# Performance work log

Hardware: AMD Instinct MI355X
Metric: run time of the kernel (lower is better)

The kernel has to match this reference:

```python
import jax, jax.numpy as jnp
import numpy as np

B, S, D_IN, D_OUT = 4, 2048, 768, 768

def setup_inputs() -> dict:
    key = jax.random.key(0)
    kx, kq, kk, kv = jax.random.split(key, 4)
    scale = 1.0 / np.sqrt(D_IN)
    return {
        "x": jax.random.normal(kx, (B, S, D_IN), dtype=jnp.float32),
        "Wq": jax.random.normal(kq, (D_OUT, D_IN), dtype=jnp.float32) * scale,
        "Wk": jax.random.normal(kk, (D_OUT, D_IN), dtype=jnp.float32) * scale,
        "Wv": jax.random.normal(kv, (D_OUT, D_IN), dtype=jnp.float32) * scale,
    }

def reference(x, Wq, Wk, Wv):
    # torch Linear: y = x @ W.T  (W is [d_out, d_in])
    q = jnp.einsum('bsd,od->bso', x, Wq)
    k = jnp.einsum('bsd,od->bso', x, Wk)
    v = jnp.einsum('bsd,od->bso', x, Wv)
    scores = jnp.einsum('bqo,bko->bqk', q, k)  # [B,S,S]
    causal = jnp.tril(jnp.ones((scores.shape[1], scores.shape[2]), dtype=bool))
    neg_inf = jnp.array(-jnp.inf, dtype=scores.dtype)
    scores = jnp.where(causal, scores, neg_inf)
    inv_sqrt_d = jnp.asarray(1.0 / np.sqrt(q.shape[-1]), dtype=scores.dtype)
    weights = jax.nn.softmax(scores * inv_sqrt_d, axis=-1)
    # dropout p=0.0 -> identity
    return jnp.einsum('bqk,bko->bqo', weights, v)
```

## Files before the change

kernel.cpp:

```cpp
#include <hip/hip_runtime.h>
#include <hip/hip_bf16.h>
#include <cstdint>
#include <cstddef>


typedef __attribute__((ext_vector_type(8))) short short8;
typedef __attribute__((ext_vector_type(4))) float f32x4;

#define GPTR(p) (const __attribute__((address_space(1))) void*)(p)
#define LPTR(p) (__attribute__((address_space(3))) void*)(p)
#define MFMA16(a8, b8, c) c = __builtin_amdgcn_mfma_f32_16x16x32_bf16(a8, b8, c, 0, 0, 0)

constexpr int CB = 4, CS = 2048, CD = 768;
constexpr int CBS = CB * CS;

typedef const __attribute__((address_space(3))) char* lds_cp;

__device__ __forceinline__ short8 ds_read128(const __hip_bfloat16* p) {
    short8 r;
    lds_cp a = (lds_cp)p;
    asm volatile("ds_read_b128 %0, %1" : "=v"(r) : "v"(a));
    return r;
}

__device__ inline unsigned short f2bf_bits(float v) {
    __hip_bfloat16 h = __float2bfloat16(v);
    unsigned short u;
    __builtin_memcpy(&u, &h, 2);
    return u;
}

__device__ inline ushort4 cvt4(float4 f) {
    ushort4 u;
    u.x = f2bf_bits(f.x); u.y = f2bf_bits(f.y);
    u.z = f2bf_bits(f.z); u.w = f2bf_bits(f.w);
    return u;
}

template <int MI>
__device__ __forceinline__ void zero_acc(f32x4 (&acc)[MI][4]) {
#pragma unroll
    for (int i = 0; i < MI; ++i)
#pragma unroll
        for (int j = 0; j < 4; ++j)
            acc[i][j] = f32x4{0.f, 0.f, 0.f, 0.f};
}

__global__ __launch_bounds__(256) void cvt_all(
    const float4* __restrict__ x,  const float4* __restrict__ wq,
    const float4* __restrict__ wk, const float4* __restrict__ wv,
    ushort4* __restrict__ x16, ushort4* __restrict__ w16,
    float4* __restrict__ rsum4)
{
    constexpr int NX = CBS * CD / 4;
    constexpr int NW = CD * CD / 4;
    constexpr int NT = NX + 3 * NW;
    const int i = blockIdx.x * 256 + threadIdx.x;
    if (i < NX) {
        x16[i] = cvt4(x[i]);
    } else if (i < NT) {
        const int j = i - NX;
        if (j < NW)            w16[j] = cvt4(wq[j]);
        else if (j < 2 * NW)   w16[j] = cvt4(wk[j - NW]);
        else                   w16[j] = cvt4(wv[j - 2 * NW]);
    } else {
        const int j = i - NT;
        rsum4[j] = float4{0.f, 0.f, 0.f, 0.f};
    }
}

__device__ __forceinline__ void gemm256_core(
    const __hip_bfloat16* __restrict__ A,
    const __hip_bfloat16* __restrict__ B,
    __hip_bfloat16* As, __hip_bfloat16* Bs,
    int m0, int n0, int K, int nkt,
    f32x4 (&acc)[8][4])
{
    const int t   = threadIdx.x;
    const int w   = t >> 6;
    const int l   = t & 63;
    const int lq  = l >> 4;
    const int lm  = l & 15;
    const int wm  = w >> 2;
    const int wn  = w & 3;
    const int lm7 = lm & 7;
    const int c0  = (lq ^ lm7) << 3;
    const int c1  = c0 ^ 32;

    const int rr0   = t >> 3;
    const int gp8   = (t & 7) << 3;
    const int g8    = (((t & 7) ^ (rr0 & 7)) << 3);
    const int rowBa = ((rr0 & 32) << 1) | (rr0 & 31);

    const __hip_bfloat16* Aori = A + (size_t)m0 * K;
    const __hip_bfloat16* Bori = B + (size_t)n0 * K;

    auto stage = [&](int reg, int bufT, int kt) {
        const int kc = kt * 64 + g8;
        const __hip_bfloat16* s0;
        __hip_bfloat16* d;
        if (reg == 0) {
            s0 = Aori + (size_t)rr0 * K + kc;
            d  = As + bufT * 16384 + rr0 * 64 + gp8;
        } else if (reg == 2) {
            s0 = Aori + (size_t)(64 + rr0) * K + kc;
            d  = As + bufT * 16384 + (64 + rr0) * 64 + gp8;
        } else if (reg == 3) {
            s0 = Bori + (size_t)rowBa * K + kc;
            d  = Bs + bufT * 16384 + rowBa * 64 + gp8;
        } else {
            s0 = Bori + (size_t)(32 + rowBa) * K + kc;
            d  = Bs + bufT * 16384 + (32 + rowBa) * 64 + gp8;
        }
        __builtin_amdgcn_global_load_lds(GPTR(s0), LPTR(d), 16, 0, 0);
        __builtin_amdgcn_global_load_lds(GPTR(s0 + (size_t)128 * K), LPTR(d + 8192), 16, 0, 0);
    };

    stage(0, 0, 0); stage(1, 0, 0); stage(2, 0, 0); stage(3, 0, 0);
    stage(0, 1, 1); stage(1, 1, 1); stage(2, 1, 1);
    asm volatile("s_waitcnt vmcnt(6)" ::: "memory");
    __builtin_amdgcn_s_barrier();

    for (int kt = 0; kt < nkt; ++kt) {
        const int buf = kt & 1;
        const __hip_bfloat16* Ab = As + buf * 16384 + wm * 8192 + lm * 64;
        const __hip_bfloat16* Bb = Bs + buf * 16384 + (wn >> 1) * 8192 + (wn & 1) * 4096 + lm * 64;
        short8 af[4][2], bf[2][2];

#pragma unroll
        for (int i = 0; i < 4; ++i) {
            af[i][0] = ds_read128(&Ab[i * 1024 + c0]);
            af[i][1] = ds_read128(&Ab[i * 1024 + c1]);
        }
#pragma unroll
        for (int j = 0; j < 2; ++j) {
            bf[j][0] = ds_read128(&Bb[j * 1024 + c0]);
            bf[j][1] = ds_read128(&Bb[j * 1024 + c1]);
        }
        if (kt + 1 < nkt) stage(3, buf ^ 1, kt + 1);
        __builtin_amdgcn_s_barrier();
        asm volatile("s_waitcnt lgkmcnt(0)");
        __builtin_amdgcn_sched_barrier(0);
        __builtin_amdgcn_s_setprio(1);
#pragma unroll
        for (int i = 0; i < 4; ++i)
#pragma unroll
            for (int j = 0; j < 2; ++j) {
                MFMA16(af[i][0], bf[j][0], acc[i][j]);
                MFMA16(af[i][1], bf[j][1], acc[i][j]);
            }
        __builtin_amdgcn_s_setprio(0);
        __builtin_amdgcn_s_barrier();

#pragma unroll
        for (int j = 0; j < 2; ++j) {
            bf[j][0] = ds_read128(&Bb[(2 + j) * 1024 + c0]);
            bf[j][1] = ds_read128(&Bb[(2 + j) * 1024 + c1]);
        }
        if (kt + 2 < nkt) stage(0, buf, kt + 2);
        __builtin_amdgcn_s_barrier();
        asm volatile("s_waitcnt lgkmcnt(0)");
        __builtin_amdgcn_sched_barrier(0);
        __builtin_amdgcn_s_setprio(1);
#pragma unroll
        for (int i = 0; i < 4; ++i)
#pragma unroll
            for (int j = 0; j < 2; ++j) {
                MFMA16(af[i][0], bf[j][0], acc[i][2 + j]);
                MFMA16(af[i][1], bf[j][1], acc[i][2 + j]);
            }
        __builtin_amdgcn_s_setprio(0);
        __builtin_amdgcn_s_barrier();

#pragma unroll
        for (int i = 0; i < 4; ++i) {
            af[i][0] = ds_read128(&Ab[(4 + i) * 1024 + c0]);
            af[i][1] = ds_read128(&Ab[(4 + i) * 1024 + c1]);
        }
        if (kt + 2 < nkt) stage(1, buf, kt + 2);
        __builtin_amdgcn_s_barrier();
        asm volatile("s_waitcnt lgkmcnt(0)");
        __builtin_amdgcn_sched_barrier(0);
        __builtin_amdgcn_s_setprio(1);
#pragma unroll
        for (int i = 0; i < 4; ++i)
#pragma unroll
            for (int j = 0; j < 2; ++j) {
                MFMA16(af[i][0], bf[j][0], acc[4 + i][2 + j]);
                MFMA16(af[i][1], bf[j][1], acc[4 + i][2 + j]);
            }
        __builtin_amdgcn_s_setprio(0);
        __builtin_amdgcn_s_barrier();

#pragma unroll
        for (int j = 0; j < 2; ++j) {
            bf[j][0] = ds_read128(&Bb[j * 1024 + c0]);
            bf[j][1] = ds_read128(&Bb[j * 1024 + c1]);
        }
        if (kt + 2 < nkt) stage(2, buf, kt + 2);
        __builtin_amdgcn_s_barrier();
        asm volatile("s_waitcnt lgkmcnt(0)");
        __builtin_amdgcn_sched_barrier(0);
        __builtin_amdgcn_s_setprio(1);
#pragma unroll
        for (int i = 0; i < 4; ++i)
#pragma unroll
            for (int j = 0; j < 2; ++j) {
                MFMA16(af[i][0], bf[j][0], acc[4 + i][j]);
                MFMA16(af[i][1], bf[j][1], acc[4 + i][j]);
            }
        __builtin_amdgcn_s_setprio(0);
        if (kt + 2 < nkt) {
            asm volatile("s_waitcnt vmcnt(6)" ::: "memory");
        } else if (kt + 1 < nkt) {
            asm volatile("s_waitcnt vmcnt(0)" ::: "memory");
        }
        __builtin_amdgcn_s_barrier();
    }
}

__global__ __launch_bounds__(512, 2) void qk256_gemm(
    const __hip_bfloat16* __restrict__ x16,
    const __hip_bfloat16* __restrict__ w16,
    __hip_bfloat16* __restrict__ q16,
    __hip_bfloat16* __restrict__ k16)
{
    __shared__ __align__(16) __hip_bfloat16 As[2 * 16384];
    __shared__ __align__(16) __hip_bfloat16 Bs[2 * 16384];

    const int id   = blockIdx.x;
    const int mi   = id / 6;
    const int r    = id % 6;
    const int proj = r / 3;
    const int nj   = r % 3;
    const int m0 = mi * 256, n0 = nj * 256;

    f32x4 acc[8][4];
    zero_acc<8>(acc);
    gemm256_core(x16, w16 + (size_t)proj * CD * CD, As, Bs, m0, n0, CD, CD / 64, acc);

    __hip_bfloat16* C = proj ? k16 : q16;
    const int t = threadIdx.x, w = t >> 6, l = t & 63, lq = l >> 4, lm = l & 15;
    const int wm = w >> 2, wn = w & 3;
#pragma unroll
    for (int i = 0; i < 8; ++i)
#pragma unroll
        for (int j = 0; j < 4; ++j) {
            const int n = n0 + wn * 64 + j * 16 + lm;
#pragma unroll
            for (int r2 = 0; r2 < 4; ++r2) {
                const int m = m0 + wm * 128 + i * 16 + lq * 4 + r2;
                C[(size_t)m * CD + n] = __float2bfloat16(acc[i][j][r2]);
            }
        }
}

__global__ __launch_bounds__(512, 2) void scores_vt_gemm(
    const __hip_bfloat16* __restrict__ q16,
    const __hip_bfloat16* __restrict__ k16,
    const __hip_bfloat16* __restrict__ x16,
    const __hip_bfloat16* __restrict__ w16,
    __hip_bfloat16* __restrict__ sp16,
    __hip_bfloat16* __restrict__ vt16,
    float* __restrict__ rowsum,
    float scale)
{
    __shared__ __align__(16) __hip_bfloat16 As[2 * 16384];
    __shared__ __align__(16) __hip_bfloat16 Bs[2 * 16384];

    const int id = blockIdx.x;
    const __hip_bfloat16 *A, *B;
    int m0, n0, b;
    const bool is_sc = (id < 144);
    if (is_sc) {
        b = id / 36;
        const int tt = id % 36;
        int mi = (int)((sqrtf(8.f * tt + 1.f) - 1.f) * 0.5f);
        while ((mi + 1) * (mi + 2) / 2 <= tt) ++mi;
        while (mi * (mi + 1) / 2 > tt) --mi;
        const int nj = tt - mi * (mi + 1) / 2;
        m0 = mi * 256; n0 = nj * 256;
        A = q16 + (size_t)b * CS * CD;
        B = k16 + (size_t)b * CS * CD;
    } else {
        int r = id - 144;
        b = r / 24; r %= 24;
        m0 = (r >> 3) * 256;
        n0 = (r & 7) * 256;
        A = w16 + (size_t)2 * CD * CD;
        B = x16 + (size_t)b * CS * CD;
    }

    f32x4 acc[8][4];
    zero_acc<8>(acc);
    gemm256_core(A, B, As, Bs, m0, n0, CD, CD / 64, acc);

    const int t = threadIdx.x, w = t >> 6, l = t & 63, lq = l >> 4, lm = l & 15;
    const int wm = w >> 2, wn = w & 3;

    if (is_sc) {
        __hip_bfloat16* C = sp16 + (size_t)b * CS * CS;
        float* rs = rowsum + (size_t)b * CS;
#pragma unroll
        for (int i = 0; i < 8; ++i) {
            float psum[4] = {0.f, 0.f, 0.f, 0.f};
#pragma unroll
            for (int j = 0; j < 4; ++j) {
                const int n = n0 + wn * 64 + j * 16 + lm;
#pragma unroll
                for (int r2 = 0; r2 < 4; ++r2) {
                    const int m = m0 + wm * 128 + i * 16 + lq * 4 + r2;
                    float e = (n <= m) ? __expf(acc[i][j][r2] * scale) : 0.f;
                    C[(size_t)m * CS + n] = __float2bfloat16(e);
                    psum[r2] += e;
                }
            }
#pragma unroll
            for (int r2 = 0; r2 < 4; ++r2) {
#pragma unroll
                for (int off = 1; off < 16; off <<= 1)
                    psum[r2] += __shfl_xor(psum[r2], off);
                if (lm == 0) {
                    const int m = m0 + wm * 128 + i * 16 + lq * 4 + r2;
                    atomicAdd(&rs[m], psum[r2]);
                }
            }
        }
    } else {
        __hip_bfloat16* C = vt16 + (size_t)b * CD * CS;
#pragma unroll
        for (int i = 0; i < 8; ++i)
#pragma unroll
            for (int j = 0; j < 4; ++j) {
                const int n = n0 + wn * 64 + j * 16 + lm;
#pragma unroll
                for (int r2 = 0; r2 < 4; ++r2) {
                    const int m = m0 + wm * 128 + i * 16 + lq * 4 + r2;
                    C[(size_t)m * CS + n] = __float2bfloat16(acc[i][j][r2]);
                }
            }
    }
}

template <int BM>
__device__ __forceinline__ void gemm_core(
    const __hip_bfloat16* __restrict__ A,
    const __hip_bfloat16* __restrict__ B,
    __hip_bfloat16* As, __hip_bfloat16* Bs,
    int m0, int n0, int K, int kend,
    f32x4 (&acc)[BM / 32][4])
{
    constexpr int AC = BM / 16;
    constexpr int SC = AC + 8;
    constexpr int MI = BM / 32;

    const int t  = threadIdx.x;
    const int w  = t >> 6;
    const int l  = t & 63;
    const int lq = l >> 4;
    const int lm = l & 15;
    const int wm = (w >> 1) * (BM / 2);
    const int wn = (w & 1) * 64;

    const int srow = l >> 2;
    const int scol = (l & 3) * 8;

    auto stage = [&](int buf, int k0) {
#pragma unroll
        for (int ci = 0; ci < SC / 4; ++ci) {
            const int c = ci * 4 + w;
            if (c < AC) {
                __builtin_amdgcn_global_load_lds(
                    GPTR(A + (size_t)(m0 + c * 16 + srow) * K + k0 + scol),
                    LPTR(&As[buf * BM * 32 + c * 512]), 16, 0, 0);
            } else {
                const int c2 = c - AC;
                __builtin_amdgcn_global_load_lds(
                    GPTR(B + (size_t)(n0 + c2 * 16 + srow) * K + k0 + scol),
                    LPTR(&Bs[buf * 128 * 32 + c2 * 512]), 16, 0, 0);
            }
        }
    };

    stage(0, 0);
    asm volatile("s_waitcnt vmcnt(0)" ::: "memory");
    __syncthreads();

    int cur = 0;
    for (int k0 = 0; k0 < kend; k0 += 32) {
        if (k0 + 32 < kend)
            stage(cur ^ 1, k0 + 32);

        short8 af[MI], bf[4];
#pragma unroll
        for (int i = 0; i < MI; ++i)
            af[i] = *(const short8*)&As[cur * BM * 32 + (wm + i * 16 + lm) * 32 + lq * 8];
#pragma unroll
        for (int j = 0; j < 4; ++j)
            bf[j] = *(const short8*)&Bs[cur * 128 * 32 + (wn + j * 16 + lm) * 32 + lq * 8];

#pragma unroll
        for (int i = 0; i < MI; ++i)
#pragma unroll
            for (int j = 0; j < 4; ++j)
                acc[i][j] = __builtin_amdgcn_mfma_f32_16x16x32_bf16(
                    af[i], bf[j], acc[i][j], 0, 0, 0);

        __syncthreads();
        cur ^= 1;
    }
}

__global__ __launch_bounds__(256) void pv_gemm(
    const __hip_bfloat16* __restrict__ sp16,
    const __hip_bfloat16* __restrict__ vt16,
    const float* __restrict__ rowsum,
    float* __restrict__ out)
{
    const int id   = blockIdx.x;
    const int mrev = id / 24;
    int r          = id % 24;
    const int b    = r / 6;
    const int n0   = (r % 6) * 128;
    const int mi   = 31 - mrev;
    const int m0   = mi * 64;
    const int kend = m0 + 64;

    __shared__ __align__(16) __hip_bfloat16 As[2 * 64 * 32];
    __shared__ __align__(16) __hip_bfloat16 Bs[2 * 128 * 32];

    const __hip_bfloat16* A = sp16 + (size_t)b * CS * CS;
    const __hip_bfloat16* B = vt16 + (size_t)b * CD * CS;
    float* Co = out + (size_t)b * CS * CD;
    const float* rs = rowsum + (size_t)b * CS;

    f32x4 acc[2][4];
    zero_acc<2>(acc);
    gemm_core<64>(A, B, As, Bs, m0, n0, CS, kend, acc);

    const int t  = threadIdx.x;
    const int w  = t >> 6;
    const int l  = t & 63;
    const int lq = l >> 4;
    const int lm = l & 15;
    const int wm = (w >> 1) * 32;
    const int wn = (w & 1) * 64;

#pragma unroll
    for (int i = 0; i < 2; ++i) {
        float inv[4];
#pragma unroll
        for (int r2 = 0; r2 < 4; ++r2)
            inv[r2] = 1.0f / rs[m0 + wm + i * 16 + lq * 4 + r2];
#pragma unroll
        for (int j = 0; j < 4; ++j) {
            const int n = n0 + wn + j * 16 + lm;
#pragma unroll
            for (int r2 = 0; r2 < 4; ++r2) {
                const int m = m0 + wm + i * 16 + lq * 4 + r2;
                Co[(size_t)m * CD + n] = acc[i][j][r2] * inv[r2];
            }
        }
    }
}

extern "C" void kernel_launch(void* const* d_in, const int* in_sizes, int n_in,
                              void* d_out, int out_size, void* d_ws, size_t ws_size,
                              hipStream_t stream)
{
    const float* x  = (const float*)d_in[0];
    const float* Wq = (const float*)d_in[1];
    const float* Wk = (const float*)d_in[2];
    const float* Wv = (const float*)d_in[3];
    float* out = (float*)d_out;

    char* ws = (char*)d_ws;
    size_t off = 0;
    auto alloc = [&](size_t bytes) { char* p = ws + off; off += bytes; return p; };

    __hip_bfloat16* x16  = (__hip_bfloat16*)alloc((size_t)CBS * CD * 2);
    __hip_bfloat16* q16  = (__hip_bfloat16*)alloc((size_t)CBS * CD * 2);
    __hip_bfloat16* k16  = (__hip_bfloat16*)alloc((size_t)CBS * CD * 2);
    __hip_bfloat16* vt16 = (__hip_bfloat16*)alloc((size_t)CBS * CD * 2);
    __hip_bfloat16* sp16 = (__hip_bfloat16*)alloc((size_t)CB * CS * CS * 2);
    __hip_bfloat16* w16  = (__hip_bfloat16*)alloc((size_t)3 * CD * CD * 2);
    float*          rsum = (float*)alloc((size_t)CB * CS * sizeof(float));

    constexpr int NCVT_BLK = (CBS * CD + 3 * CD * CD) / 4 / 256 + 8;
    cvt_all<<<NCVT_BLK, 256, 0, stream>>>(
        (const float4*)x, (const float4*)Wq, (const float4*)Wk, (const float4*)Wv,
        (ushort4*)x16, (ushort4*)w16, (float4*)rsum);

    qk256_gemm<<<192, 512, 0, stream>>>(x16, w16, q16, k16);

    scores_vt_gemm<<<240, 512, 0, stream>>>(
        q16, k16, x16, w16, sp16, vt16, rsum, 0.03608439182435161f);

    pv_gemm<<<768, 256, 0, stream>>>(sp16, vt16, rsum, out);
}
```

Measured before the change: 181.5 us.

## Replace PV GEMM with 256-tile split-K kernel using atomics and XCD swizzle

Replaces the 64x128-tile PV kernel with a 256x256-tile kernel that reuses the pipelined gemm256_core. Causal K ranges are split into chunks of 8 k-tiles, and the partial results are combined with float atomicAdd into an output zeroed by an added memset. XCD-aware block swizzling is also applied to the earlier GEMM kernels to improve L2 locality. This trades more data reuse per tile and a balanced 240-block grid for atomic traffic, a memset pass, and nondeterministic summation order.

```diff
diff --git a/kernel.cpp b/kernel.cpp
--- a/kernel.cpp
+++ b/kernel.cpp
@@ -21,6 +21,10 @@
     lds_cp a = (lds_cp)p;
     asm volatile("ds_read_b128 %0, %1" : "=v"(r) : "v"(a));
     return r;
+}
+
+__device__ __forceinline__ int xcd_swz(int bid, int nwg) {
+    return (bid & 7) * (nwg >> 3) + (bid >> 3);
 }
 
 __device__ inline unsigned short f2bf_bits(float v) {
@@ -228,7 +232,7 @@
     __shared__ __align__(16) __hip_bfloat16 As[2 * 16384];
     __shared__ __align__(16) __hip_bfloat16 Bs[2 * 16384];
 
-    const int id   = blockIdx.x;
+    const int id   = xcd_swz(blockIdx.x, 192);
     const int mi   = id / 6;
     const int r    = id % 6;
     const int proj = r / 3;
@@ -268,7 +272,7 @@
     __shared__ __align__(16) __hip_bfloat16 As[2 * 16384];
     __shared__ __align__(16) __hip_bfloat16 Bs[2 * 16384];
 
-    const int id = blockIdx.x;
+    const int id = xcd_swz(blockIdx.x, 240);
     const __hip_bfloat16 *A, *B;
     int m0, n0, b;
     const bool is_sc = (id < 144);
@@ -342,123 +346,53 @@
     }
 }
 
-template <int BM>
-__device__ __forceinline__ void gemm_core(
-    const __hip_bfloat16* __restrict__ A,
-    const __hip_bfloat16* __restrict__ B,
-    __hip_bfloat16* As, __hip_bfloat16* Bs,
-    int m0, int n0, int K, int kend,
-    f32x4 (&acc)[BM / 32][4])
-{
-    constexpr int AC = BM / 16;
-    constexpr int SC = AC + 8;
-    constexpr int MI = BM / 32;
-
-    const int t  = threadIdx.x;
-    const int w  = t >> 6;
-    const int l  = t & 63;
-    const int lq = l >> 4;
-    const int lm = l & 15;
-    const int wm = (w >> 1) * (BM / 2);
-    const int wn = (w & 1) * 64;
-
-    const int srow = l >> 2;
-    const int scol = (l & 3) * 8;
-
-    auto stage = [&](int buf, int k0) {
-#pragma unroll
-        for (int ci = 0; ci < SC / 4; ++ci) {
-            const int c = ci * 4 + w;
-            if (c < AC) {
-                __builtin_amdgcn_global_load_lds(
-                    GPTR(A + (size_t)(m0 + c * 16 + srow) * K + k0 + scol),
-                    LPTR(&As[buf * BM * 32 + c * 512]), 16, 0, 0);
-            } else {
-                const int c2 = c - AC;
-                __builtin_amdgcn_global_load_lds(
-                    GPTR(B + (size_t)(n0 + c2 * 16 + srow) * K + k0 + scol),
-                    LPTR(&Bs[buf * 128 * 32 + c2 * 512]), 16, 0, 0);
-            }
-        }
-    };
-
-    stage(0, 0);
-    asm volatile("s_waitcnt vmcnt(0)" ::: "memory");
-    __syncthreads();
-
-    int cur = 0;
-    for (int k0 = 0; k0 < kend; k0 += 32) {
-        if (k0 + 32 < kend)
-            stage(cur ^ 1, k0 + 32);
-
-        short8 af[MI], bf[4];
-#pragma unroll
-        for (int i = 0; i < MI; ++i)
-            af[i] = *(const short8*)&As[cur * BM * 32 + (wm + i * 16 + lm) * 32 + lq * 8];
-#pragma unroll
-        for (int j = 0; j < 4; ++j)
-            bf[j] = *(const short8*)&Bs[cur * 128 * 32 + (wn + j * 16 + lm) * 32 + lq * 8];
-
-#pragma unroll
-        for (int i = 0; i < MI; ++i)
-#pragma unroll
-            for (int j = 0; j < 4; ++j)
-                acc[i][j] = __builtin_amdgcn_mfma_f32_16x16x32_bf16(
-                    af[i], bf[j], acc[i][j], 0, 0, 0);
-
-        __syncthreads();
-        cur ^= 1;
-    }
-}
-
-__global__ __launch_bounds__(256) void pv_gemm(
+__global__ __launch_bounds__(512, 2) void pv256_gemm(
     const __hip_bfloat16* __restrict__ sp16,
     const __hip_bfloat16* __restrict__ vt16,
     const float* __restrict__ rowsum,
     float* __restrict__ out)
 {
-    const int id   = blockIdx.x;
-    const int mrev = id / 24;
-    int r          = id % 24;
-    const int b    = r / 6;
-    const int n0   = (r % 6) * 128;
-    const int mi   = 31 - mrev;
-    const int m0   = mi * 64;
-    const int kend = m0 + 64;
-
-    __shared__ __align__(16) __hip_bfloat16 As[2 * 64 * 32];
-    __shared__ __align__(16) __hip_bfloat16 Bs[2 * 128 * 32];
-
-    const __hip_bfloat16* A = sp16 + (size_t)b * CS * CS;
-    const __hip_bfloat16* B = vt16 + (size_t)b * CD * CS;
+    __shared__ __align__(16) __hip_bfloat16 As[2 * 16384];
+    __shared__ __align__(16) __hip_bfloat16 Bs[2 * 16384];
+
+    const int id    = xcd_swz(blockIdx.x, 240);
+    const int panel = id / 20;
+    int c           = id % 20;
+    const int b  = panel / 3;
+    const int nj = panel % 3;
+    int mi = 0;
+    while (c >= (mi >> 1) + 1) { c -= (mi >> 1) + 1; ++mi; }
+    const int kt0 = c * 8;
+    const int nkt = min(8, 4 * (mi + 1) - kt0);
+    const int m0 = mi * 256, n0 = nj * 256;
+
+    const __hip_bfloat16* A = sp16 + (size_t)b * CS * CS + kt0 * 64;
+    const __hip_bfloat16* B = vt16 + (size_t)b * CD * CS + kt0 * 64;
+
+    f32x4 acc[8][4];
+    zero_acc<8>(acc);
+    gemm256_core(A, B, As, Bs, m0, n0, CS, nkt, acc);
+
     float* Co = out + (size_t)b * CS * CD;
     const float* rs = rowsum + (size_t)b * CS;
-
-    f32x4 acc[2][4];
-    zero_acc<2>(acc);
-    gemm_core<64>(A, B, As, Bs, m0, n0, CS, kend, acc);
-
-    const int t  = threadIdx.x;
-    const int w  = t >> 6;
-    const int l  = t & 63;
-    const int lq = l >> 4;
-    const int lm = l & 15;
-    const int wm = (w >> 1) * 32;
-    const int wn = (w & 1) * 64;
-
-#pragma unroll
-    for (int i = 0; i < 2; ++i) {
+    const int t = threadIdx.x, w = t >> 6, l = t & 63, lq = l >> 4, lm = l & 15;
+    const int wm = w >> 2, wn = w & 3;
+    const bool single = (mi < 2);
+#pragma unroll
+    for (int i = 0; i < 8; ++i) {
         float inv[4];
 #pragma unroll
         for (int r2 = 0; r2 < 4; ++r2)
-            inv[r2] = 1.0f / rs[m0 + wm + i * 16 + lq * 4 + r2];
+            inv[r2] = 1.0f / rs[m0 + wm * 128 + i * 16 + lq * 4 + r2];
 #pragma unroll
         for (int j = 0; j < 4; ++j) {
-            const int n = n0 + wn + j * 16 + lm;
+            const int n = n0 + wn * 64 + j * 16 + lm;
 #pragma unroll
             for (int r2 = 0; r2 < 4; ++r2) {
-                const int m = m0 + wm + i * 16 + lq * 4 + r2;
-                Co[(size_t)m * CD + n] = acc[i][j][r2] * inv[r2];
+                const int m = m0 + wm * 128 + i * 16 + lq * 4 + r2;
+                const float v = acc[i][j][r2] * inv[r2];
+                if (single) Co[(size_t)m * CD + n] = v;
+                else        atomicAdd(&Co[(size_t)m * CD + n], v);
             }
         }
     }
@@ -486,6 +420,8 @@
     __hip_bfloat16* w16  = (__hip_bfloat16*)alloc((size_t)3 * CD * CD * 2);
     float*          rsum = (float*)alloc((size_t)CB * CS * sizeof(float));
 
+    hipMemsetAsync(out, 0, (size_t)CBS * CD * sizeof(float), stream);
+
     constexpr int NCVT_BLK = (CBS * CD + 3 * CD * CD) / 4 / 256 + 8;
     cvt_all<<<NCVT_BLK, 256, 0, stream>>>(
         (const float4*)x, (const float4*)Wq, (const float4*)Wk, (const float4*)Wv,
@@ -496,5 +432,5 @@
     scores_vt_gemm<<<240, 512, 0, stream>>>(
         q16, k16, x16, w16, sp16, vt16, rsum, 0.03608439182435161f);
 
-    pv_gemm<<<768, 256, 0, stream>>>(sp16, vt16, rsum, out);
-}
+    pv256_gemm<<<240, 512, 0, stream>>>(sp16, vt16, rsum, out);
+}
```

After: 201.8 us. 1.11x slower.

## Hold both A and B fragment halves in registers and swizzle blocks across XCDs

Applied to the files above, without the earlier changes.

The GEMM inner loop now loads both B half-fragments up front and keeps the low and high A fragments in separate registers. This removes the repeated B reloads and one LDS read phase with its barriers per k-tile, and a partial lgkmcnt wait lets the first MFMA block start before all reads finish. Block IDs in both GEMM kernels are also remapped so that neighbouring tiles land on the same XCD, aiming for better L2 reuse. The cost is higher register pressure from the extra fragment arrays, which could hurt occupancy at 512 threads with a minimum of 2 blocks per CU. The last phase also drops a barrier around its staging, which may be fragile.

```diff
diff --git a/kernel.cpp b/kernel.cpp
--- a/kernel.cpp
+++ b/kernel.cpp
@@ -21,6 +21,10 @@
     lds_cp a = (lds_cp)p;
     asm volatile("ds_read_b128 %0, %1" : "=v"(r) : "v"(a));
     return r;
+}
+
+__device__ __forceinline__ int xcd_swz(int bid, int nwg) {
+    return (bid & 7) * (nwg >> 3) + (bid >> 3);
 }
 
 __device__ inline unsigned short f2bf_bits(float v) {
@@ -125,19 +129,40 @@
         const int buf = kt & 1;
         const __hip_bfloat16* Ab = As + buf * 16384 + wm * 8192 + lm * 64;
         const __hip_bfloat16* Bb = Bs + buf * 16384 + (wn >> 1) * 8192 + (wn & 1) * 4096 + lm * 64;
-        short8 af[4][2], bf[2][2];
+        short8 alo[4][2], ahi[4][2], ba[2][2], bb[2][2];
 
 #pragma unroll
         for (int i = 0; i < 4; ++i) {
-            af[i][0] = ds_read128(&Ab[i * 1024 + c0]);
-            af[i][1] = ds_read128(&Ab[i * 1024 + c1]);
+            alo[i][0] = ds_read128(&Ab[i * 1024 + c0]);
+            alo[i][1] = ds_read128(&Ab[i * 1024 + c1]);
         }
 #pragma unroll
         for (int j = 0; j < 2; ++j) {
-            bf[j][0] = ds_read128(&Bb[j * 1024 + c0]);
-            bf[j][1] = ds_read128(&Bb[j * 1024 + c1]);
-        }
+            ba[j][0] = ds_read128(&Bb[j * 1024 + c0]);
+            ba[j][1] = ds_read128(&Bb[j * 1024 + c1]);
+        }
+#pragma unroll
+        for (int j = 0; j < 2; ++j) {
+            bb[j][0] = ds_read128(&Bb[(2 + j) * 1024 + c0]);
+            bb[j][1] = ds_read128(&Bb[(2 + j) * 1024 + c1]);
+        }
+
         if (kt + 1 < nkt) stage(3, buf ^ 1, kt + 1);
+        __builtin_amdgcn_s_barrier();
+        asm volatile("s_waitcnt lgkmcnt(4)");
+        __builtin_amdgcn_sched_barrier(0);
+        __builtin_amdgcn_s_setprio(1);
+#pragma unroll
+        for (int i = 0; i < 4; ++i)
+#pragma unroll
+            for (int j = 0; j < 2; ++j) {
+                MFMA16(alo[i][0], ba[j][0], acc[i][j]);
+                MFMA16(alo[i][1], ba[j][1], acc[i][j]);
+            }
+        __builtin_amdgcn_s_setprio(0);
+        __builtin_amdgcn_s_barrier();
+
+        if (kt + 2 < nkt) stage(0, buf, kt + 2);
         __builtin_amdgcn_s_barrier();
         asm volatile("s_waitcnt lgkmcnt(0)");
         __builtin_amdgcn_sched_barrier(0);
@@ -146,18 +171,18 @@
         for (int i = 0; i < 4; ++i)
 #pragma unroll
             for (int j = 0; j < 2; ++j) {
-                MFMA16(af[i][0], bf[j][0], acc[i][j]);
-                MFMA16(af[i][1], bf[j][1], acc[i][j]);
+                MFMA16(alo[i][0], bb[j][0], acc[i][2 + j]);
+                MFMA16(alo[i][1], bb[j][1], acc[i][2 + j]);
             }
         __builtin_amdgcn_s_setprio(0);
         __builtin_amdgcn_s_barrier();
 
 #pragma unroll
-        for (int j = 0; j < 2; ++j) {
-            bf[j][0] = ds_read128(&Bb[(2 + j) * 1024 + c0]);
-            bf[j][1] = ds_read128(&Bb[(2 + j) * 1024 + c1]);
-        }
-        if (kt + 2 < nkt) stage(0, buf, kt + 2);
+        for (int i = 0; i < 4; ++i) {
+            ahi[i][0] = ds_read128(&Ab[(4 + i) * 1024 + c0]);
+            ahi[i][1] = ds_read128(&Ab[(4 + i) * 1024 + c1]);
+        }
+        if (kt + 2 < nkt) stage(1, buf, kt + 2);
         __builtin_amdgcn_s_barrier();
         asm volatile("s_waitcnt lgkmcnt(0)");
         __builtin_amdgcn_sched_barrier(0);
@@ -166,48 +191,20 @@
         for (int i = 0; i < 4; ++i)
 #pragma unroll
             for (int j = 0; j < 2; ++j) {
-                MFMA16(af[i][0], bf[j][0], acc[i][2 + j]);
-                MFMA16(af[i][1], bf[j][1], acc[i][2 + j]);
+                MFMA16(ahi[i][0], bb[j][0], acc[4 + i][2 + j]);
+                MFMA16(ahi[i][1], bb[j][1], acc[4 + i][2 + j]);
             }
         __builtin_amdgcn_s_setprio(0);
         __builtin_amdgcn_s_barrier();
 
-#pragma unroll
-        for (int i = 0; i < 4; ++i) {
-            af[i][0] = ds_read128(&Ab[(4 + i) * 1024 + c0]);
-            af[i][1] = ds_read128(&Ab[(4 + i) * 1024 + c1]);
-        }
-        if (kt + 2 < nkt) stage(1, buf, kt + 2);
-        __builtin_amdgcn_s_barrier();
-        asm volatile("s_waitcnt lgkmcnt(0)");
-        __builtin_amdgcn_sched_barrier(0);
+        if (kt + 2 < nkt) stage(2, buf, kt + 2);
         __builtin_amdgcn_s_setprio(1);
 #pragma unroll
         for (int i = 0; i < 4; ++i)
 #pragma unroll
             for (int j = 0; j < 2; ++j) {
-                MFMA16(af[i][0], bf[j][0], acc[4 + i][2 + j]);
-                MFMA16(af[i][1], bf[j][1], acc[4 + i][2 + j]);
-            }
-        __builtin_amdgcn_s_setprio(0);
-        __builtin_amdgcn_s_barrier();
-
-#pragma unroll
-        for (int j = 0; j < 2; ++j) {
-            bf[j][0] = ds_read128(&Bb[j * 1024 + c0]);
-            bf[j][1] = ds_read128(&Bb[j * 1024 + c1]);
-        }
-        if (kt + 2 < nkt) stage(2, buf, kt + 2);
-        __builtin_amdgcn_s_barrier();
-        asm volatile("s_waitcnt lgkmcnt(0)");
-        __builtin_amdgcn_sched_barrier(0);
-        __builtin_amdgcn_s_setprio(1);
-#pragma unroll
-        for (int i = 0; i < 4; ++i)
-#pragma unroll
-            for (int j = 0; j < 2; ++j) {
-                MFMA16(af[i][0], bf[j][0], acc[4 + i][j]);
-                MFMA16(af[i][1], bf[j][1], acc[4 + i][j]);
+                MFMA16(ahi[i][0], ba[j][0], acc[4 + i][j]);
+                MFMA16(ahi[i][1], ba[j][1], acc[4 + i][j]);
             }
         __builtin_amdgcn_s_setprio(0);
         if (kt + 2 < nkt) {
@@ -228,7 +225,7 @@
     __shared__ __align__(16) __hip_bfloat16 As[2 * 16384];
     __shared__ __align__(16) __hip_bfloat16 Bs[2 * 16384];
 
-    const int id   = blockIdx.x;
+    const int id   = xcd_swz(blockIdx.x, 192);
     const int mi   = id / 6;
     const int r    = id % 6;
     const int proj = r / 3;
@@ -268,7 +265,7 @@
     __shared__ __align__(16) __hip_bfloat16 As[2 * 16384];
     __shared__ __align__(16) __hip_bfloat16 Bs[2 * 16384];
 
-    const int id = blockIdx.x;
+    const int id = xcd_swz(blockIdx.x, 240);
     const __hip_bfloat16 *A, *B;
     int m0, n0, b;
     const bool is_sc = (id < 144);
```

Result: no change. 179.0 us (-1.4%).
